# Performance work log

Measured on AMD Instinct MI355X. Metric: run time of the kernel, lower is better.

## Reference

```python
import jax, jax.numpy as jnp
import numpy as np

NUM_HEADS = 12
HEAD_DIM = 64
SCALE = HEAD_DIM ** -0.5


def setup_inputs() -> dict:
    key = jax.random.key(0)
    ks = jax.random.split(key, 6)
    B, N, C = 32, 577, 768
    x = jax.random.normal(ks[0], (B, N, C), dtype=jnp.float32)
    w_qkv = jax.random.normal(ks[1], (3 * C, C), dtype=jnp.float32) * (C ** -0.5)
    w_proj = jax.random.normal(ks[2], (C, C), dtype=jnp.float32) * (C ** -0.5)
    b_proj = jnp.zeros((C,), dtype=jnp.float32)
    # RoPE tables for the N-1 patch tokens, per rotation pair (head_dim//2)
    ang = jax.random.uniform(ks[3], (N - 1, HEAD_DIM // 2), dtype=jnp.float32) * (2 * np.pi)
    cos = jnp.cos(ang)
    sin = jnp.sin(ang)
    return {"x": x, "w_qkv": w_qkv, "w_proj": w_proj, "b_proj": b_proj, "cos": cos, "sin": sin}


def _rotate(t, cos, sin):
    # t: [B,H,P,D]; cos/sin: [P,D/2] broadcast to [1,1,P,D/2]
    t1 = t[..., 0::2]
    t2 = t[..., 1::2]
    c = cos[None, None]
    s = sin[None, None]
    r1 = t1 * c - t2 * s
    r2 = t1 * s + t2 * c
    return jnp.stack([r1, r2], axis=-1).reshape(t.shape)


def reference(x, w_qkv, w_proj, b_proj, cos, sin):
    B, N, C = x.shape
    H, D = NUM_HEADS, HEAD_DIM
    qkv = (x @ w_qkv.T).reshape(B, N, 3, H, D)
    qkv = jnp.transpose(qkv, (2, 0, 3, 1, 4))  # [3,B,H,N,D]
    q, k, v = qkv[0], qkv[1], qkv[2]
    # RoPE on patch tokens only; CLS token (index 0) left unrotated
    q = jnp.concatenate([q[:, :, :1], _rotate(q[:, :, 1:], cos, sin)], axis=2)
    k = jnp.concatenate([k[:, :, :1], _rotate(k[:, :, 1:], cos, sin)], axis=2)
    attn = jnp.einsum("bhqd,bhkd->bhqk", q, k) * SCALE
    attn = jax.nn.softmax(attn, axis=-1)
    out = jnp.einsum("bhqk,bhkd->bhqd", attn, v)
    out = jnp.transpose(out, (0, 2, 1, 3)).reshape(B, N, C)
    return out @ w_proj.T + b_proj
```

## Files before the change

kernel.cpp:

```cpp
#include <hip/hip_runtime.h>


#define M_ROWS 18464
#define M_PAD  18560
#define CDIM   768
#define QKVN   2304
#define NHEADS 12
#define BHEADS 384
#define NSEQ   577
#define NPAD   640
#define SCALE  0.125f

typedef __bf16 bf16x8 __attribute__((ext_vector_type(8)));
typedef __bf16 bf16x4 __attribute__((ext_vector_type(4)));
typedef float  f32x4  __attribute__((ext_vector_type(4)));

typedef const __attribute__((address_space(1))) void* gas_ptr;
typedef __attribute__((address_space(3))) void* las_ptr;

__device__ inline void gload16(const __bf16* g, __bf16* l) {
  __builtin_amdgcn_global_load_lds((gas_ptr)g, (las_ptr)l, 16, 0, 0);
}

__device__ inline int xcd_swizzle(int orig, int nwg) {
  int q = nwg >> 3, r = nwg & 7;
  int xcd = orig & 7, idx = orig >> 3;
  int base = (xcd < r) ? xcd * (q + 1) : r * (q + 1) + (xcd - r) * q;
  return base + idx;
}


__global__ void cvt_pad(const float* __restrict__ src, __bf16* __restrict__ dst,
                        long n_src, long n_dst) {
  long i = ((long)blockIdx.x * 256 + threadIdx.x) * 4;
  if (i >= n_dst) return;
  if (i + 3 < n_src) {
    f32x4 v = *(const f32x4*)(src + i);
    bf16x4 o = {(__bf16)v[0], (__bf16)v[1], (__bf16)v[2], (__bf16)v[3]};
    *(bf16x4*)(dst + i) = o;
  } else {
#pragma unroll
    for (int j = 0; j < 4; j++)
      if (i + j < n_dst) dst[i + j] = (i + j < n_src) ? (__bf16)src[i + j] : (__bf16)0.0f;
  }
}

__global__ void pad_zero(__bf16* __restrict__ q, __bf16* __restrict__ k) {
  int i = blockIdx.x * 256 + threadIdx.x;
  if (i >= BHEADS * 63 * 64) return;
  int d = i & 63;
  int t = i >> 6;
  int sp = t % 63, bh = t / 63;
  int s = NSEQ + sp;
  q[((size_t)bh * NPAD + s) * 64 + d] = (__bf16)0.0f;
  k[((size_t)bh * NPAD + s) * 64 + d] = (__bf16)0.0f;
}


#define G1_NWG (18 * 145)

__launch_bounds__(256, 2)
__global__ void gemm1(const __bf16* __restrict__ A, const __bf16* __restrict__ Bw,
                      __bf16* __restrict__ qq, __bf16* __restrict__ kk,
                      __bf16* __restrict__ vr,
                      const float* __restrict__ cs, const float* __restrict__ sn) {
  __shared__ __bf16 smem[3 * 4096 * 2];
  const int wgid = xcd_swizzle(blockIdx.x, G1_NWG);
  const int bn = wgid % 18, bm = wgid / 18;
  const int tid = threadIdx.x;
  const int w = tid >> 6, lane = tid & 63;
  const int lr = lane & 15, quad = lane >> 4;
  const int r0 = tid >> 2;
  const int kq = (tid & 3) * 8;
  const int K = CDIM;

  f32x4 acc[4][4] = {};
  const __bf16* Ab = A + (size_t)(bm * 128 + r0) * K + kq;
  const __bf16* Bb = Bw + (size_t)(bn * 128 + r0) * K + kq;
  const int wm = (w >> 1) * 64, wn = (w & 1) * 64;

  auto stage = [&](int kt, int buf) __attribute__((always_inline)) {
    gload16(Ab + kt, &smem[buf * 4096 + tid * 8]);
    gload16(Ab + kt + 64 * K, &smem[buf * 4096 + tid * 8 + 2048]);
    gload16(Bb + kt, &smem[12288 + buf * 4096 + tid * 8]);
    gload16(Bb + kt + 64 * K, &smem[12288 + buf * 4096 + tid * 8 + 2048]);
  };

  stage(0, 0);
  stage(32, 1);
  asm volatile("s_waitcnt vmcnt(4)" ::: "memory");
  asm volatile("s_barrier" ::: "memory");

  int c0 = 0, c1 = 1, c2 = 2;
#pragma unroll 1
  for (int kt = 0; kt < K; kt += 32) {
    if (kt + 64 < K) stage(kt + 64, c2);

    bf16x8 af[4], bfr[4];
#pragma unroll
    for (int i = 0; i < 4; i++) {
      af[i]  = *(const bf16x8*)&smem[c0 * 4096 + (wm + i * 16 + lr) * 32 + quad * 8];
      bfr[i] = *(const bf16x8*)&smem[12288 + c0 * 4096 + (wn + i * 16 + lr) * 32 + quad * 8];
    }
#pragma unroll
    for (int i = 0; i < 4; i++)
#pragma unroll
      for (int j = 0; j < 4; j++)
        acc[i][j] = __builtin_amdgcn_mfma_f32_16x16x32_bf16(af[i], bfr[j], acc[i][j], 0, 0, 0);

    if (kt + 64 < K)      asm volatile("s_waitcnt vmcnt(4)" ::: "memory");
    else if (kt + 32 < K) asm volatile("s_waitcnt vmcnt(0)" ::: "memory");
    asm volatile("s_barrier" ::: "memory");

    int tmp = c0; c0 = c1; c1 = c2; c2 = tmp;
  }

  __syncthreads();
  __bf16* tile = smem;
  const bool isv = (bn >= 12);

#pragma unroll
  for (int i = 0; i < 4; i++) {
#pragma unroll
    for (int r = 0; r < 4; r++) {
      int ml = wm + i * 16 + quad * 4 + r;
      int m = bm * 128 + ml;
      int s = 0;
      if (!isv) { int b = m / NSEQ; s = m - b * NSEQ; }
#pragma unroll
      for (int j = 0; j < 4; j++) {
        int nl = wn + j * 16 + lr;
        float v = acc[i][j][r];
        float outv = v;
        if (!isv) {
          float pv = __shfl_xor(v, 1, 64);
          if (s >= 1 && m < M_ROWS) {
            int d = nl & 63;
            float c  = cs[(size_t)(s - 1) * 32 + (d >> 1)];
            float sv = sn[(size_t)(s - 1) * 32 + (d >> 1)];
            outv = (nl & 1) ? (pv * sv + v * c) : (v * c - pv * sv);
          }
        }
        tile[ml * 136 + nl] = (__bf16)outv;
      }
    }
  }
  __syncthreads();

  {
    const int tq = tid >> 4, tc = tid & 15;
    const int t_blk = bn / 6;
    const int bnq = bn % 6;
    __bf16* dstb = (t_blk == 0) ? qq : (t_blk == 1) ? kk : vr;
    const int SS = (t_blk == 2) ? NSEQ : NPAD;
    const int h = bnq * 2 + (tc >> 3);
    const int d0 = (tc & 7) * 8;
#pragma unroll
    for (int p = 0; p < 8; p++) {
      int ml = p * 16 + tq;
      int m = bm * 128 + ml;
      if (m < M_ROWS) {
        int b = m / NSEQ, s = m - b * NSEQ;
        bf16x8 val = *(const bf16x8*)&tile[ml * 136 + tc * 8];
        *(bf16x8*)&dstb[(((size_t)(b * NHEADS + h) * SS + s) << 6) + d0] = val;
      }
    }
  }
}


__global__ void vtrans(const __bf16* __restrict__ vr, __bf16* __restrict__ vt) {
  __shared__ __bf16 t[64 * 72];
  int blk = blockIdx.x;
  int bh = blk / 10, sc = blk % 10;
  int tid = threadIdx.x;
  int ts = tid >> 2;
  int dc = (tid & 3) * 16;
  int s = sc * 64 + ts;
  bf16x8 a = {}, b2 = {};
  if (s < NSEQ) {
    const __bf16* src = vr + ((size_t)bh * NSEQ + s) * 64 + dc;
    a  = *(const bf16x8*)src;
    b2 = *(const bf16x8*)(src + 8);
  }
#pragma unroll
  for (int e = 0; e < 8; e++) {
    t[(dc + e) * 72 + ts]     = a[e];
    t[(dc + 8 + e) * 72 + ts] = b2[e];
  }
  __syncthreads();
  int d = tid >> 2;
  int scol = (tid & 3) * 16;
  bf16x8 o0 = *(const bf16x8*)&t[d * 72 + scol];
  bf16x8 o1 = *(const bf16x8*)&t[d * 72 + scol + 8];
  __bf16* dst = vt + ((size_t)bh * 64 + d) * NPAD + sc * 64 + scol;
  *(bf16x8*)dst = o0;
  *(bf16x8*)(dst + 8) = o1;
}


#define AT_NWG (BHEADS * 5)

__launch_bounds__(256, 3)
__global__ void attn(const __bf16* __restrict__ q, const __bf16* __restrict__ k,
                     const __bf16* __restrict__ vT, __bf16* __restrict__ aoh) {
  __shared__ float Xf[4][1152];
  const int blk = xcd_swizzle(blockIdx.x, AT_NWG);
  const int qt5 = blk % 5, bh = blk / 5;
  const int b = bh / NHEADS, h = bh % NHEADS;
  const int w = threadIdx.x >> 6, lane = threadIdx.x & 63;
  const int lr = lane & 15, quad = lane >> 4;
  const int qbase = qt5 * 128 + w * 32;

  float* xw = &Xf[w][0];
  __bf16* pw = (__bf16*)xw;

  bf16x8 qf[2][2];
#pragma unroll
  for (int qt = 0; qt < 2; qt++)
#pragma unroll
    for (int kh = 0; kh < 2; kh++)
      qf[qt][kh] = *(const bf16x8*)(q + ((size_t)bh * NPAD + qbase + qt * 16 + lr) * 64 + kh * 32 + quad * 8);

  f32x4 O[2][4] = {};
  float l_p[2] = {0.0f, 0.0f};
  const float C1 = SCALE * 1.44269504089f;
  const float C0 = -8.0f * 1.44269504089f;
  const __bf16* kbase = k + (size_t)bh * NPAD * 64;
  const __bf16* vbase = vT + (size_t)bh * 64 * NPAD;

  auto tile = [&](int kv0, bool masked) __attribute__((always_inline)) {
    bf16x8 kf[4][2];
#pragma unroll
    for (int nt = 0; nt < 4; nt++)
#pragma unroll
      for (int kh = 0; kh < 2; kh++)
        kf[nt][kh] = *(const bf16x8*)(kbase + (size_t)(kv0 + nt * 16 + lr) * 64 + kh * 32 + quad * 8);

    f32x4 st[2][4];
#pragma unroll
    for (int qt = 0; qt < 2; qt++)
#pragma unroll
      for (int nt = 0; nt < 4; nt++) {
        f32x4 z = {};
        z = __builtin_amdgcn_mfma_f32_16x16x32_bf16(kf[nt][0], qf[qt][0], z, 0, 0, 0);
        z = __builtin_amdgcn_mfma_f32_16x16x32_bf16(kf[nt][1], qf[qt][1], z, 0, 0, 0);
        st[qt][nt] = z;
      }

    bf16x8 vf[4][2];
#pragma unroll
    for (int nt2 = 0; nt2 < 4; nt2++)
#pragma unroll
      for (int kt = 0; kt < 2; kt++)
        vf[nt2][kt] = *(const bf16x8*)(vbase + (size_t)(nt2 * 16 + lr) * NPAD + kv0 + kt * 32 + quad * 8);

#pragma unroll
    for (int qt = 0; qt < 2; qt++) {
      float rs = 0.0f;
#pragma unroll
      for (int nt = 0; nt < 4; nt++) {
        f32x4 pv;
#pragma unroll
        for (int r = 0; r < 4; r++) {
          float p = __builtin_amdgcn_exp2f(st[qt][nt][r] * C1 + C0);
          if (masked && !(nt == 0 && quad == 0 && r == 0)) p = 0.0f;
          pv[r] = p;
        }
        rs += pv[0] + pv[1] + pv[2] + pv[3];
        bf16x4 pk = {(__bf16)pv[0], (__bf16)pv[1], (__bf16)pv[2], (__bf16)pv[3]};
        *(bf16x4*)&pw[qt * 1152 + lr * 72 + nt * 16 + quad * 4] = pk;
      }
      l_p[qt] += rs;
    }

    bf16x8 pf[2][2];
#pragma unroll
    for (int qt = 0; qt < 2; qt++)
#pragma unroll
      for (int kt = 0; kt < 2; kt++)
        pf[qt][kt] = *(const bf16x8*)&pw[qt * 1152 + lr * 72 + kt * 32 + quad * 8];

#pragma unroll
    for (int qt = 0; qt < 2; qt++)
#pragma unroll
      for (int nt2 = 0; nt2 < 4; nt2++) {
        O[qt][nt2] = __builtin_amdgcn_mfma_f32_16x16x32_bf16(vf[nt2][0], pf[qt][0], O[qt][nt2], 0, 0, 0);
        O[qt][nt2] = __builtin_amdgcn_mfma_f32_16x16x32_bf16(vf[nt2][1], pf[qt][1], O[qt][nt2], 0, 0, 0);
      }
  };

#pragma unroll 1
  for (int it = 0; it < 9; it++) tile(it * 64, false);
  tile(576, true);

#pragma unroll
  for (int qt = 0; qt < 2; qt++) {
    float lf = l_p[qt];
    lf += __shfl_xor(lf, 16, 64);
    lf += __shfl_xor(lf, 32, 64);
    float inv = 1.0f / lf;
#pragma unroll
    for (int nt2 = 0; nt2 < 4; nt2++) {
      f32x4 t;
#pragma unroll
      for (int r = 0; r < 4; r++) t[r] = O[qt][nt2][r] * inv;
      *(f32x4*)&xw[lr * 68 + nt2 * 16 + quad * 4] = t;
    }
#pragma unroll
    for (int p = 0; p < 4; p++) {
      int lm = p * 4 + quad;
      int s = qbase + qt * 16 + lm;
      if (s < NSEQ) {
        f32x4 t = *(const f32x4*)&xw[lm * 68 + lr * 4];
        bf16x4 hi;
#pragma unroll
        for (int r = 0; r < 4; r++) hi[r] = (__bf16)t[r];
        size_t base = ((size_t)b * NSEQ + s) * CDIM + h * 64 + lr * 4;
        *(bf16x4*)&aoh[base] = hi;
      }
    }
  }
}


#define G2_NWG (6 * 145)

__launch_bounds__(256, 2)
__global__ void gemm2(const __bf16* __restrict__ A, const __bf16* __restrict__ Bw,
                      const float* __restrict__ bias, float* __restrict__ out) {
  __shared__ __bf16 As[3][128 * 32];
  __shared__ __bf16 Bs[3][128 * 32];
  const int wgid = xcd_swizzle(blockIdx.x, G2_NWG);
  const int bn = wgid % 6, bm = wgid / 6;
  const int tid = threadIdx.x;
  const int w = tid >> 6, lane = tid & 63;
  const int lr = lane & 15, quad = lane >> 4;
  const int r0 = tid >> 2;
  const int kq = (tid & 3) * 8;
  const int K = CDIM;

  f32x4 acc[4][4] = {};
  const __bf16* Ab = A + (size_t)(bm * 128 + r0) * K + kq;
  const __bf16* Bb = Bw + (size_t)(bn * 128 + r0) * K + kq;
  const int wm = (w >> 1) * 64, wn = (w & 1) * 64;

  auto stage = [&](int kt, int buf) __attribute__((always_inline)) {
    gload16(Ab + kt, &As[buf][tid * 8]);
    gload16(Ab + kt + 64 * K, &As[buf][tid * 8 + 2048]);
    gload16(Bb + kt, &Bs[buf][tid * 8]);
    gload16(Bb + kt + 64 * K, &Bs[buf][tid * 8 + 2048]);
  };

  stage(0, 0);
  stage(32, 1);
  asm volatile("s_waitcnt vmcnt(4)" ::: "memory");
  asm volatile("s_barrier" ::: "memory");

  int c0 = 0, c1 = 1, c2 = 2;
#pragma unroll 1
  for (int kt = 0; kt < K; kt += 32) {
    if (kt + 64 < K) stage(kt + 64, c2);

    bf16x8 af[4], bfr[4];
#pragma unroll
    for (int i = 0; i < 4; i++) {
      af[i]  = *(const bf16x8*)&As[c0][(wm + i * 16 + lr) * 32 + quad * 8];
      bfr[i] = *(const bf16x8*)&Bs[c0][(wn + i * 16 + lr) * 32 + quad * 8];
    }
#pragma unroll
    for (int i = 0; i < 4; i++)
#pragma unroll
      for (int j = 0; j < 4; j++)
        acc[i][j] = __builtin_amdgcn_mfma_f32_16x16x32_bf16(af[i], bfr[j], acc[i][j], 0, 0, 0);

    if (kt + 64 < K)      asm volatile("s_waitcnt vmcnt(4)" ::: "memory");
    else if (kt + 32 < K) asm volatile("s_waitcnt vmcnt(0)" ::: "memory");
    asm volatile("s_barrier" ::: "memory");

    int tmp = c0; c0 = c1; c1 = c2; c2 = tmp;
  }

#pragma unroll
  for (int i = 0; i < 4; i++)
#pragma unroll
    for (int r = 0; r < 4; r++) {
      int m = bm * 128 + wm + i * 16 + quad * 4 + r;
      if (m < M_ROWS) {
#pragma unroll
        for (int j = 0; j < 4; j++) {
          int n = bn * 128 + wn + j * 16 + lr;
          out[(size_t)m * CDIM + n] = acc[i][j][r] + bias[n];
        }
      }
    }
}


extern "C" void kernel_launch(void* const* d_in, const int* in_sizes, int n_in,
                              void* d_out, int out_size, void* d_ws, size_t ws_size,
                              hipStream_t stream) {
  const float* x      = (const float*)d_in[0];
  const float* w_qkv  = (const float*)d_in[1];
  const float* w_proj = (const float*)d_in[2];
  const float* b_proj = (const float*)d_in[3];
  const float* cosp   = (const float*)d_in[4];
  const float* sinp   = (const float*)d_in[5];
  float* out = (float*)d_out;

  char* ws = (char*)d_ws;
  auto carve = [&](size_t elts) {
    __bf16* p = (__bf16*)ws;
    ws += ((elts * 2 + 255) / 256) * 256;
    return p;
  };
  __bf16* xb    = carve((size_t)M_PAD * CDIM);
  __bf16* wqkvb = carve((size_t)QKVN * CDIM);
  __bf16* wpb   = carve((size_t)CDIM * CDIM);
  __bf16* qq    = carve((size_t)BHEADS * NPAD * 64);
  __bf16* kk    = carve((size_t)BHEADS * NPAD * 64);
  __bf16* vv    = carve((size_t)BHEADS * NPAD * 64);
  __bf16* aoh   = carve((size_t)M_PAD * CDIM);
  __bf16* vr    = aoh;

  cvt_pad<<<((M_PAD * CDIM) / 4 + 255) / 256, 256, 0, stream>>>(x, xb, (long)M_ROWS * CDIM, (long)M_PAD * CDIM);
  cvt_pad<<<((QKVN * CDIM) / 4 + 255) / 256, 256, 0, stream>>>(w_qkv, wqkvb, (long)QKVN * CDIM, (long)QKVN * CDIM);
  cvt_pad<<<((CDIM * CDIM) / 4 + 255) / 256, 256, 0, stream>>>(w_proj, wpb, (long)CDIM * CDIM, (long)CDIM * CDIM);
  pad_zero<<<(BHEADS * 63 * 64 + 255) / 256, 256, 0, stream>>>(qq, kk);
  gemm1<<<G1_NWG, 256, 0, stream>>>(xb, wqkvb, qq, kk, vr, cosp, sinp);
  vtrans<<<BHEADS * 10, 256, 0, stream>>>(vr, vv);
  attn<<<AT_NWG, 256, 0, stream>>>(qq, kk, vv, aoh);
  gemm2<<<G2_NWG, 256, 0, stream>>>(aoh, wpb, b_proj, out);
}
```

Measured before the change: 441.0 us.

## Split attention KV loop across two wave halves and merge partial outputs

The attention block grows to 512 threads: each query slice is handled by two waves, and each wave processes half of the ten key tiles. Partial O accumulators and row sums are combined through shared memory before normalisation and the output store. The aim is more parallelism per query and a shorter serial KV loop, at the cost of a shared-memory reduction, extra barriers, and tighter register limits from the new launch bounds. This relies on the softmax using a fixed max offset, so partial sums can be added directly without rescaling.

```diff
diff --git a/kernel.cpp b/kernel.cpp
--- a/kernel.cpp
+++ b/kernel.cpp
@@ -201,16 +201,17 @@
 
 #define AT_NWG (BHEADS * 5)
 
-__launch_bounds__(256, 3)
+__launch_bounds__(512, 4)
 __global__ void attn(const __bf16* __restrict__ q, const __bf16* __restrict__ k,
                      const __bf16* __restrict__ vT, __bf16* __restrict__ aoh) {
-  __shared__ float Xf[4][1152];
+  __shared__ float Xf[8][1152];
   const int blk = xcd_swizzle(blockIdx.x, AT_NWG);
   const int qt5 = blk % 5, bh = blk / 5;
   const int b = bh / NHEADS, h = bh % NHEADS;
   const int w = threadIdx.x >> 6, lane = threadIdx.x & 63;
+  const int qs = w & 3, half = w >> 2;
   const int lr = lane & 15, quad = lane >> 4;
-  const int qbase = qt5 * 128 + w * 32;
+  const int qbase = qt5 * 128 + qs * 32;
 
   float* xw = &Xf[w][0];
   __bf16* pw = (__bf16*)xw;
@@ -291,8 +292,36 @@
   };
 
 #pragma unroll 1
-  for (int it = 0; it < 9; it++) tile(it * 64, false);
-  tile(576, true);
+  for (int it = half * 5; it < half * 5 + 5; it++) tile(it * 64, it == 9);
+
+  __syncthreads();
+  float* comb = &Xf[0][0];
+  if (half == 1) {
+    float* cb = comb + qs * 2176;
+#pragma unroll
+    for (int qt = 0; qt < 2; qt++) {
+#pragma unroll
+      for (int nt2 = 0; nt2 < 4; nt2++)
+        *(f32x4*)&cb[qt * 1024 + nt2 * 256 + lane * 4] = O[qt][nt2];
+      cb[2048 + qt * 64 + lane] = l_p[qt];
+    }
+  }
+  __syncthreads();
+  if (half == 0) {
+    const float* cb = comb + qs * 2176;
+#pragma unroll
+    for (int qt = 0; qt < 2; qt++) {
+#pragma unroll
+      for (int nt2 = 0; nt2 < 4; nt2++) {
+        f32x4 t = *(const f32x4*)&cb[qt * 1024 + nt2 * 256 + lane * 4];
+#pragma unroll
+        for (int r = 0; r < 4; r++) O[qt][nt2][r] += t[r];
+      }
+      l_p[qt] += cb[2048 + qt * 64 + lane];
+    }
+  }
+  __syncthreads();
+  if (half == 1) return;
 
 #pragma unroll
   for (int qt = 0; qt < 2; qt++) {
@@ -429,6 +458,6 @@
   pad_zero<<<(BHEADS * 63 * 64 + 255) / 256, 256, 0, stream>>>(qq, kk);
   gemm1<<<G1_NWG, 256, 0, stream>>>(xb, wqkvb, qq, kk, vr, cosp, sinp);
   vtrans<<<BHEADS * 10, 256, 0, stream>>>(vr, vv);
-  attn<<<AT_NWG, 256, 0, stream>>>(qq, kk, vv, aoh);
+  attn<<<AT_NWG, 512, 0, stream>>>(qq, kk, vv, aoh);
   gemm2<<<G2_NWG, 256, 0, stream>>>(aoh, wpb, b_proj, out);
 }
```

Measured after the change: 480.6 us. 9.0% more time.

## Prefetch next K tile, raise MFMA priority, replace masked tail tile with scalar path

Applied to the files above, without the earlier changes.

The attention loop now loads the next tile's K fragments while the current tile computes softmax and PV, so global-load latency overlaps with compute. MFMA blocks are wrapped in s_setprio to favour matrix issue across waves. The last key (index 576), which used to be handled by a full masked 64-wide tile, is now computed as a scalar dot product and a rank-1 update, removing about a tenth of the attention MFMA and exp work. The cost is higher register pressure from holding the prefetched K fragments, plus some scalar-path instructions.

```diff
diff --git a/kernel.cpp b/kernel.cpp
--- a/kernel.cpp
+++ b/kernel.cpp
@@ -229,15 +229,22 @@
   const __bf16* kbase = k + (size_t)bh * NPAD * 64;
   const __bf16* vbase = vT + (size_t)bh * 64 * NPAD;
 
-  auto tile = [&](int kv0, bool masked) __attribute__((always_inline)) {
-    bf16x8 kf[4][2];
+  bf16x8 kf[4][2];
+  auto loadK = [&](int kv0) __attribute__((always_inline)) {
 #pragma unroll
     for (int nt = 0; nt < 4; nt++)
 #pragma unroll
       for (int kh = 0; kh < 2; kh++)
         kf[nt][kh] = *(const bf16x8*)(kbase + (size_t)(kv0 + nt * 16 + lr) * 64 + kh * 32 + quad * 8);
+  };
+
+  loadK(0);
+#pragma unroll 1
+  for (int it = 0; it < 9; it++) {
+    const int kv0 = it * 64;
 
     f32x4 st[2][4];
+    __builtin_amdgcn_s_setprio(1);
 #pragma unroll
     for (int qt = 0; qt < 2; qt++)
 #pragma unroll
@@ -247,6 +254,7 @@
         z = __builtin_amdgcn_mfma_f32_16x16x32_bf16(kf[nt][1], qf[qt][1], z, 0, 0, 0);
         st[qt][nt] = z;
       }
+    __builtin_amdgcn_s_setprio(0);
 
     bf16x8 vf[4][2];
 #pragma unroll
@@ -255,6 +263,8 @@
       for (int kt = 0; kt < 2; kt++)
         vf[nt2][kt] = *(const bf16x8*)(vbase + (size_t)(nt2 * 16 + lr) * NPAD + kv0 + kt * 32 + quad * 8);
 
+    if (it < 8) loadK(kv0 + 64);
+
 #pragma unroll
     for (int qt = 0; qt < 2; qt++) {
       float rs = 0.0f;
@@ -262,11 +272,8 @@
       for (int nt = 0; nt < 4; nt++) {
         f32x4 pv;
 #pragma unroll
-        for (int r = 0; r < 4; r++) {
-          float p = __builtin_amdgcn_exp2f(st[qt][nt][r] * C1 + C0);
-          if (masked && !(nt == 0 && quad == 0 && r == 0)) p = 0.0f;
-          pv[r] = p;
-        }
+        for (int r = 0; r < 4; r++)
+          pv[r] = __builtin_amdgcn_exp2f(st[qt][nt][r] * C1 + C0);
         rs += pv[0] + pv[1] + pv[2] + pv[3];
         bf16x4 pk = {(__bf16)pv[0], (__bf16)pv[1], (__bf16)pv[2], (__bf16)pv[3]};
         *(bf16x4*)&pw[qt * 1152 + lr * 72 + nt * 16 + quad * 4] = pk;
@@ -281,6 +288,7 @@
       for (int kt = 0; kt < 2; kt++)
         pf[qt][kt] = *(const bf16x8*)&pw[qt * 1152 + lr * 72 + kt * 32 + quad * 8];
 
+    __builtin_amdgcn_s_setprio(1);
 #pragma unroll
     for (int qt = 0; qt < 2; qt++)
 #pragma unroll
@@ -288,11 +296,37 @@
         O[qt][nt2] = __builtin_amdgcn_mfma_f32_16x16x32_bf16(vf[nt2][0], pf[qt][0], O[qt][nt2], 0, 0, 0);
         O[qt][nt2] = __builtin_amdgcn_mfma_f32_16x16x32_bf16(vf[nt2][1], pf[qt][1], O[qt][nt2], 0, 0, 0);
       }
-  };
-
-#pragma unroll 1
-  for (int it = 0; it < 9; it++) tile(it * 64, false);
-  tile(576, true);
+    __builtin_amdgcn_s_setprio(0);
+  }
+
+  {
+    bf16x8 k5[2];
+#pragma unroll
+    for (int kh = 0; kh < 2; kh++)
+      k5[kh] = *(const bf16x8*)(kbase + (size_t)576 * 64 + kh * 32 + quad * 8);
+    float p5[2];
+#pragma unroll
+    for (int qt = 0; qt < 2; qt++) {
+      float s = 0.0f;
+#pragma unroll
+      for (int kh = 0; kh < 2; kh++)
+#pragma unroll
+        for (int j = 0; j < 8; j++)
+          s += (float)qf[qt][kh][j] * (float)k5[kh][j];
+      s += __shfl_xor(s, 16, 64);
+      s += __shfl_xor(s, 32, 64);
+      p5[qt] = __builtin_amdgcn_exp2f(s * C1 + C0);
+      if (quad == 0) l_p[qt] += p5[qt];
+    }
+#pragma unroll
+    for (int nt2 = 0; nt2 < 4; nt2++)
+#pragma unroll
+      for (int r = 0; r < 4; r++) {
+        float vv = (float)vbase[(size_t)(nt2 * 16 + quad * 4 + r) * NPAD + 576];
+        O[0][nt2][r] += p5[0] * vv;
+        O[1][nt2][r] += p5[1] * vv;
+      }
+  }
 
 #pragma unroll
   for (int qt = 0; qt < 2; qt++) {
```

After: 428.7 us. 1.03x faster.
